# Kernel tuning notes

Hardware: AMD Instinct MI355X
Metric: run time of the kernel (lower is better)

Reference implementation:

```python
import math
import jax, jax.numpy as jnp
import numpy as np

H = 32          # query heads
KV = 8          # key/value heads (GQA)
D = 128         # head_dim
PAGE = 16       # Quest page size
TOPK = 256      # page budget
THETA = 10000.0


def _rope(x, pos):
    # x: [..., D]; llama rotate_half RoPE at scalar position pos
    half = D // 2
    inv = 1.0 / (THETA ** (jnp.arange(half, dtype=jnp.float32) * 2.0 / D))
    ang = pos * inv                                   # [half]
    cos = jnp.concatenate([jnp.cos(ang), jnp.cos(ang)])  # [D]
    sin = jnp.concatenate([jnp.sin(ang), jnp.sin(ang)])
    rot = jnp.concatenate([-x[..., half:], x[..., :half]], axis=-1)
    return x * cos + rot * sin


def setup_inputs() -> dict:
    key = jax.random.key(0)
    ks = jax.random.split(key, 7)
    hid = H * D
    s = 1.0 / math.sqrt(hid)
    return {
        "hidden_states": jax.random.normal(ks[0], (1, 1, hid), jnp.float32),
        "k_cache": jax.random.normal(ks[1], (32767, KV, D), jnp.float32),
        "v_cache": jax.random.normal(ks[2], (32767, KV, D), jnp.float32),
        "Wq": jax.random.normal(ks[3], (hid, H * D), jnp.float32) * s,
        "Wk": jax.random.normal(ks[4], (hid, KV * D), jnp.float32) * s,
        "Wv": jax.random.normal(ks[5], (hid, KV * D), jnp.float32) * s,
        "Wo": jax.random.normal(ks[6], (H * D, hid), jnp.float32) * s,
    }


def reference(hidden_states, k_cache, v_cache, Wq, Wk, Wv, Wo):
    x = hidden_states[0]                    # [1, hidden]
    q = (x @ Wq).reshape(H, D)              # decode: q_len == 1
    k = (x @ Wk).reshape(KV, D)
    v = (x @ Wv).reshape(KV, D)

    past = k_cache.shape[0]
    q = _rope(q, jnp.float32(past))
    k = _rope(k, jnp.float32(past))

    # append_kv: paged cache, seqlen = past + 1 = n_pages * PAGE
    Kc = jnp.concatenate([k_cache, k[None]], axis=0)   # [S, KV, D]
    Vc = jnp.concatenate([v_cache, v[None]], axis=0)
    S = past + 1
    n_pages = S // PAGE

    # decode_estimate: per-page min/max key metadata, Quest upper-bound score
    Kp = Kc.reshape(n_pages, PAGE, KV, D)
    kmax = Kp.max(axis=1)                   # [P, KV, D]
    kmin = Kp.min(axis=1)
    G = H // KV
    qh = q.reshape(KV, G, D)
    pmax = qh[None] * kmax[:, :, None, :]   # [P, KV, G, D]
    pmin = qh[None] * kmin[:, :, None, :]
    score = jnp.maximum(pmax, pmin).sum(-1) # [P, KV, G]
    score = score.reshape(n_pages, H).T     # [H, P]
    # most recent page always attended
    score = score.at[:, -1].set(jnp.inf)

    # decode_topk: per-head page selection
    _, pidx = jax.lax.top_k(score, TOPK)    # [H, TOPK]
    tok = (pidx[..., None] * PAGE + jnp.arange(PAGE)).reshape(H, -1)  # [H, T]

    # decode_sparse_attn: gather selected pages (GQA mapping) + attention
    kvmap = jnp.arange(H) // G              # query head -> kv head
    Ksel = Kc[tok, kvmap[:, None]]          # [H, T, D]
    Vsel = Vc[tok, kvmap[:, None]]
    att = jnp.einsum('hd,htd->ht', q, Ksel) * (1.0 / math.sqrt(D))
    w = jax.nn.softmax(att, axis=-1)
    out = jnp.einsum('ht,htd->hd', w, Vsel) # [H, D]

    y = out.reshape(1, H * D) @ Wo          # o_proj
    return y[None]                          # [1, 1, hidden]
```

## Files before the change

kernel.cpp:

```cpp
#include <hip/hip_runtime.h>
#include <math.h>

#define H 32
#define KV 8
#define D 128
#define PAGE 16
#define TOPK 256
#define NPAGES 2048
#define PAST 32767
#define HID 4096

#define WS_Q      0
#define WS_K      4096
#define WS_V      5120
#define WS_SCORES 6144
#define WS_PIDX   71680
#define WS_PART_M 79872
#define WS_PART_L 80896
#define WS_PART_O 81920
#define WS_ATTN   212992

#define NCHUNK 32
#define PPC    8

__global__ void qkv_kernel(const float* __restrict__ x,
                           const float* __restrict__ Wq,
                           const float* __restrict__ Wk,
                           const float* __restrict__ Wv,
                           float* __restrict__ ws) {
    __shared__ float xs[256];
    int tid = threadIdx.x;
    int rc = blockIdx.x / 24;
    int cg = blockIdx.x % 24;
    int r0 = rc * 256;
    xs[tid] = x[r0 + tid];
    __syncthreads();
    const float* W; int Cc; int col; float* dst;
    if (cg < 16)      { W = Wq; Cc = 4096; col = cg * 256 + tid;        dst = ws + WS_Q + col; }
    else if (cg < 20) { W = Wk; Cc = 1024; col = (cg - 16) * 256 + tid; dst = ws + WS_K + col; }
    else              { W = Wv; Cc = 1024; col = (cg - 20) * 256 + tid; dst = ws + WS_V + col; }
    const float* Wp = W + (size_t)r0 * Cc + col;
    float acc = 0.f;
#pragma unroll 8
    for (int r = 0; r < 256; ++r)
        acc = fmaf(xs[r], Wp[(size_t)r * Cc], acc);
    atomicAdd(dst, acc);
}

__global__ void rope_kernel(float* __restrict__ ws) {
    int idx = blockIdx.x * blockDim.x + threadIdx.x;
    if (idx >= 2560) return;
    float* base;
    if (idx < 2048) base = ws + WS_Q + (idx >> 6) * 128;
    else            base = ws + WS_K + ((idx - 2048) >> 6) * 128;
    int j = idx & 63;
    double t = (double)j / 64.0;
    float p = (float)pow(10000.0, t);
    float invf = 1.0f / p;
    float ang = 32767.0f * invf;
    float c = (float)cos((double)ang);
    float s = (float)sin((double)ang);
    float x0 = base[j], x1 = base[j + 64];
    base[j]      = x0 * c - x1 * s;
    base[j + 64] = x1 * c + x0 * s;
}

__global__ void score_kernel(const float* __restrict__ kc,
                             const float* __restrict__ q,
                             float* __restrict__ scores) {
    int tid = threadIdx.x;
    int lane = tid & 63;
    int wv = tid >> 6;
    int p = blockIdx.x >> 1;
    int kv = ((blockIdx.x & 1) << 2) + wv;
    const float* kp = kc + ((size_t)(p * PAGE) * KV + kv) * D + 2 * lane;
    float mx0 = -INFINITY, mx1 = -INFINITY, mn0 = INFINITY, mn1 = INFINITY;
#pragma unroll
    for (int t = 0; t < PAGE; ++t) {
        float2 v = *(const float2*)(kp + (size_t)t * (KV * D));
        mx0 = fmaxf(mx0, v.x); mn0 = fminf(mn0, v.x);
        mx1 = fmaxf(mx1, v.y); mn1 = fminf(mn1, v.y);
    }
    float sacc[4];
#pragma unroll
    for (int g = 0; g < 4; ++g) {
        int h = kv * 4 + g;
        float q0 = q[h * 128 + 2 * lane];
        float q1 = q[h * 128 + 2 * lane + 1];
        sacc[g] = fmaxf(q0 * mx0, q0 * mn0) + fmaxf(q1 * mx1, q1 * mn1);
    }
#pragma unroll
    for (int off = 32; off > 0; off >>= 1) {
#pragma unroll
        for (int g = 0; g < 4; ++g) sacc[g] += __shfl_xor(sacc[g], off);
    }
    if (lane == 0) {
#pragma unroll
        for (int g = 0; g < 4; ++g)
            scores[(size_t)(kv * 4 + g) * NPAGES + p] = sacc[g];
    }
}

__global__ void topk_kernel(const float* __restrict__ scores, int* __restrict__ pidx) {
    __shared__ unsigned su[NPAGES];
    __shared__ int hist[256];
    __shared__ int scan[256];
    __shared__ int wtot[4];
    __shared__ int cnt;
    __shared__ unsigned s_prefix;
    __shared__ int s_k;
    int tid = threadIdx.x;
    int lane = tid & 63;
    int wv = tid >> 6;
    int h = blockIdx.x;
    for (int i = tid; i < NPAGES; i += 256) {
        unsigned u;
        if (i == NPAGES - 1) u = 0xFFFFFFFFu;
        else {
            int b = __float_as_int(scores[(size_t)h * NPAGES + i]);
            u = (b >= 0) ? ((unsigned)b | 0x80000000u) : ~(unsigned)b;
        }
        su[i] = u;
    }
    if (tid == 0) cnt = 0;
    __syncthreads();

    unsigned prefix = 0;
    int K = TOPK;
    for (int level = 3; level >= 0; --level) {
        int shift = level * 8;
        unsigned pmask = (level == 3) ? 0u : (0xFFFFFFFFu << (shift + 8));
        hist[tid] = 0;
        __syncthreads();
        for (int i = tid; i < NPAGES; i += 256) {
            unsigned u = su[i];
            if ((u & pmask) == prefix)
                atomicAdd(&hist[(u >> shift) & 0xFF], 1);
        }
        __syncthreads();
        int v = hist[tid];
#pragma unroll
        for (int off = 1; off < 64; off <<= 1) {
            int o = __shfl_down(v, off);
            if (lane + off < 64) v += o;
        }
        if (lane == 0) wtot[wv] = v;
        __syncthreads();
        int add = 0;
        for (int w2 = wv + 1; w2 < 4; ++w2) add += wtot[w2];
        v += add;
        scan[tid] = v;
        __syncthreads();
        int nxt = (tid < 255) ? scan[tid + 1] : 0;
        if (v >= K && nxt < K) {
            s_prefix = prefix | ((unsigned)tid << shift);
            s_k = K - nxt;
        }
        __syncthreads();
        prefix = s_prefix;
        K = s_k;
        __syncthreads();
    }
    unsigned T = prefix;

    for (int i = tid; i < NPAGES; i += 256) {
        if (su[i] > T) {
            int pos = atomicAdd(&cnt, 1);
            pidx[h * TOPK + pos] = i;
        }
    }
    int base = TOPK - K;
    int i0 = tid * (NPAGES / 256);
    int tcount = 0;
#pragma unroll
    for (int j = 0; j < NPAGES / 256; ++j) if (su[i0 + j] == T) ++tcount;
    int sc = tcount;
#pragma unroll
    for (int off = 1; off < 64; off <<= 1) {
        int o = __shfl_up(sc, off);
        if (lane >= off) sc += o;
    }
    __syncthreads();
    if (lane == 63) wtot[wv] = sc;
    __syncthreads();
    int wadd = 0;
    for (int w2 = 0; w2 < wv; ++w2) wadd += wtot[w2];
    int pos = base + (sc - tcount) + wadd;
#pragma unroll
    for (int j = 0; j < NPAGES / 256; ++j) {
        if (su[i0 + j] == T) {
            if (pos < TOPK) pidx[h * TOPK + pos] = i0 + j;
            ++pos;
        }
    }
}

__global__ void attn_kernel(const float* __restrict__ kc,
                            const float* __restrict__ vc,
                            const float* __restrict__ ws,
                            const int* __restrict__ pidx,
                            float* __restrict__ part_m,
                            float* __restrict__ part_l,
                            float* __restrict__ part_o) {
    int tid = threadIdx.x;
    int lane = tid & 63;
    int wv = tid >> 6;
    int h = blockIdx.x >> 5;
    int c = blockIdx.x & 31;
    int kvh = h >> 2;
    __shared__ float qs[128];
    __shared__ float sm[4], sl[4];
    __shared__ float so[4 * 128];
    if (tid < 128) qs[tid] = ws[WS_Q + h * 128 + tid];
    __syncthreads();
    float q0 = qs[2 * lane], q1 = qs[2 * lane + 1];
    float m = -INFINITY, l = 0.f, o0 = 0.f, o1 = 0.f;
    const float scale = 0.08838834764831843f;
    for (int pi = 0; pi < 2; ++pi) {
        int page = pidx[h * TOPK + c * PPC + wv * 2 + pi];
        for (int t = 0; t < PAGE; ++t) {
            int tok = page * PAGE + t;
            const float *kp, *vp;
            if (tok == PAST) { kp = ws + WS_K + kvh * 128; vp = ws + WS_V + kvh * 128; }
            else {
                size_t off = ((size_t)tok * KV + kvh) * D;
                kp = kc + off; vp = vc + off;
            }
            float2 kk = *(const float2*)(kp + 2 * lane);
            float s = q0 * kk.x + q1 * kk.y;
#pragma unroll
            for (int off2 = 32; off2 > 0; off2 >>= 1) s += __shfl_xor(s, off2);
            s *= scale;
            float2 vvv = *(const float2*)(vp + 2 * lane);
            float nm = fmaxf(m, s);
            float rs = expf(m - nm);
            float w = expf(s - nm);
            l = l * rs + w;
            o0 = o0 * rs + w * vvv.x;
            o1 = o1 * rs + w * vvv.y;
            m = nm;
        }
    }
    if (lane == 0) { sm[wv] = m; sl[wv] = l; }
    so[wv * 128 + 2 * lane]     = o0;
    so[wv * 128 + 2 * lane + 1] = o1;
    __syncthreads();
    if (tid < 128) {
        float M = fmaxf(fmaxf(sm[0], sm[1]), fmaxf(sm[2], sm[3]));
        float L = 0.f, O = 0.f;
#pragma unroll
        for (int w2 = 0; w2 < 4; ++w2) {
            float f = expf(sm[w2] - M);
            L += f * sl[w2];
            O += f * so[w2 * 128 + tid];
        }
        int pc = h * NCHUNK + c;
        if (tid == 0) { part_m[pc] = M; part_l[pc] = L; }
        part_o[(size_t)pc * 128 + tid] = O;
    }
}

__global__ void combine_kernel(const float* __restrict__ part_m,
                               const float* __restrict__ part_l,
                               const float* __restrict__ part_o,
                               float* __restrict__ attn) {
    int h = blockIdx.x;
    int d = threadIdx.x;
    float M = -INFINITY;
    for (int c = 0; c < NCHUNK; ++c) M = fmaxf(M, part_m[h * NCHUNK + c]);
    float L = 0.f, O = 0.f;
    for (int c = 0; c < NCHUNK; ++c) {
        float f = expf(part_m[h * NCHUNK + c] - M);
        L += f * part_l[h * NCHUNK + c];
        O += f * part_o[(size_t)(h * NCHUNK + c) * 128 + d];
    }
    attn[h * 128 + d] = O / L;
}

__global__ void wo_kernel(const float* __restrict__ attn,
                          const float* __restrict__ Wo,
                          float* __restrict__ out) {
    __shared__ float xs[256];
    int tid = threadIdx.x;
    int rc = blockIdx.x >> 4;
    int cb = blockIdx.x & 15;
    int r0 = rc * 256;
    xs[tid] = attn[r0 + tid];
    __syncthreads();
    int col = cb * 256 + tid;
    const float* Wp = Wo + (size_t)r0 * 4096 + col;
    float acc = 0.f;
#pragma unroll 8
    for (int r = 0; r < 256; ++r)
        acc = fmaf(xs[r], Wp[(size_t)r * 4096], acc);
    atomicAdd(out + col, acc);
}

extern "C" void kernel_launch(void* const* d_in, const int* in_sizes, int n_in,
                              void* d_out, int out_size, void* d_ws, size_t ws_size,
                              hipStream_t stream) {
    const float* x  = (const float*)d_in[0];
    const float* kc = (const float*)d_in[1];
    const float* vc = (const float*)d_in[2];
    const float* Wq = (const float*)d_in[3];
    const float* Wk = (const float*)d_in[4];
    const float* Wv = (const float*)d_in[5];
    const float* Wo = (const float*)d_in[6];
    float* ws = (float*)d_ws;
    float* out = (float*)d_out;

    hipMemsetAsync(ws, 0, 6144 * sizeof(float), stream);
    hipMemsetAsync(out, 0, (size_t)out_size * sizeof(float), stream);

    qkv_kernel<<<384, 256, 0, stream>>>(x, Wq, Wk, Wv, ws);
    rope_kernel<<<10, 256, 0, stream>>>(ws);
    score_kernel<<<(NPAGES - 1) * 2, 256, 0, stream>>>(kc, ws + WS_Q, ws + WS_SCORES);
    topk_kernel<<<H, 256, 0, stream>>>(ws + WS_SCORES, (int*)(ws + WS_PIDX));
    attn_kernel<<<H * NCHUNK, 256, 0, stream>>>(kc, vc, ws, (const int*)(ws + WS_PIDX),
                                                ws + WS_PART_M, ws + WS_PART_L, ws + WS_PART_O);
    combine_kernel<<<H, 128, 0, stream>>>(ws + WS_PART_M, ws + WS_PART_L, ws + WS_PART_O,
                                          ws + WS_ATTN);
    wo_kernel<<<256, 256, 0, stream>>>(ws + WS_ATTN, Wo, out);
}
```

Measured before the change: 411.9 us.

## Vectorize GEMV, score and attention loads to float4 with restructured work split

The QKV and o_proj GEMV kernels switch to float4 weight loads, with each thread computing four columns over 64-row chunks, which changes the block decomposition. The score kernel reads keys as float4, with two half-waves covering alternate tokens that are merged by shuffle. The attention kernel gives each half-wave one page and replaces the online softmax with a two-pass score-then-accumulate over 16 tokens, combining 8 partials per block. The aim is wider memory transactions and shorter serial dependency chains, at the cost of more atomics per block and more registers. The launch configuration is not shown, so the grid sizes must match the new 6x64 and 4x64 block layouts.

```diff
diff --git a/kernel.cpp b/kernel.cpp
--- a/kernel.cpp
+++ b/kernel.cpp
@@ -28,23 +28,32 @@
                            const float* __restrict__ Wk,
                            const float* __restrict__ Wv,
                            float* __restrict__ ws) {
-    __shared__ float xs[256];
-    int tid = threadIdx.x;
-    int rc = blockIdx.x / 24;
-    int cg = blockIdx.x % 24;
-    int r0 = rc * 256;
-    xs[tid] = x[r0 + tid];
+    __shared__ float xs[64];
+    int tid = threadIdx.x;
+    int rc = blockIdx.x / 6;
+    int cg = blockIdx.x % 6;
+    int r0 = rc * 64;
+    if (tid < 64) xs[tid] = x[r0 + tid];
     __syncthreads();
     const float* W; int Cc; int col; float* dst;
-    if (cg < 16)      { W = Wq; Cc = 4096; col = cg * 256 + tid;        dst = ws + WS_Q + col; }
-    else if (cg < 20) { W = Wk; Cc = 1024; col = (cg - 16) * 256 + tid; dst = ws + WS_K + col; }
-    else              { W = Wv; Cc = 1024; col = (cg - 20) * 256 + tid; dst = ws + WS_V + col; }
+    if (cg < 4)       { W = Wq; Cc = 4096; col = cg * 1024 + tid * 4; dst = ws + WS_Q + col; }
+    else if (cg == 4) { W = Wk; Cc = 1024; col = tid * 4;             dst = ws + WS_K + col; }
+    else              { W = Wv; Cc = 1024; col = tid * 4;             dst = ws + WS_V + col; }
     const float* Wp = W + (size_t)r0 * Cc + col;
-    float acc = 0.f;
+    float4 acc = {0.f, 0.f, 0.f, 0.f};
 #pragma unroll 8
-    for (int r = 0; r < 256; ++r)
-        acc = fmaf(xs[r], Wp[(size_t)r * Cc], acc);
-    atomicAdd(dst, acc);
+    for (int r = 0; r < 64; ++r) {
+        float4 w4 = *(const float4*)(Wp + (size_t)r * Cc);
+        float xr = xs[r];
+        acc.x = fmaf(xr, w4.x, acc.x);
+        acc.y = fmaf(xr, w4.y, acc.y);
+        acc.z = fmaf(xr, w4.z, acc.z);
+        acc.w = fmaf(xr, w4.w, acc.w);
+    }
+    atomicAdd(dst + 0, acc.x);
+    atomicAdd(dst + 1, acc.y);
+    atomicAdd(dst + 2, acc.z);
+    atomicAdd(dst + 3, acc.w);
 }
 
 __global__ void rope_kernel(float* __restrict__ ws) {
@@ -71,26 +80,35 @@
     int tid = threadIdx.x;
     int lane = tid & 63;
     int wv = tid >> 6;
+    int sub = lane & 31;
+    int hf = lane >> 5;
     int p = blockIdx.x >> 1;
     int kv = ((blockIdx.x & 1) << 2) + wv;
-    const float* kp = kc + ((size_t)(p * PAGE) * KV + kv) * D + 2 * lane;
-    float mx0 = -INFINITY, mx1 = -INFINITY, mn0 = INFINITY, mn1 = INFINITY;
-#pragma unroll
-    for (int t = 0; t < PAGE; ++t) {
-        float2 v = *(const float2*)(kp + (size_t)t * (KV * D));
-        mx0 = fmaxf(mx0, v.x); mn0 = fminf(mn0, v.x);
-        mx1 = fmaxf(mx1, v.y); mn1 = fminf(mn1, v.y);
-    }
+    const float* kp0 = kc + ((size_t)(p * PAGE) * KV + kv) * D + 4 * sub;
+    float4 mx = {-INFINITY, -INFINITY, -INFINITY, -INFINITY};
+    float4 mn = { INFINITY,  INFINITY,  INFINITY,  INFINITY};
+#pragma unroll
+    for (int s8 = 0; s8 < 8; ++s8) {
+        int t = 2 * s8 + hf;
+        float4 v = *(const float4*)(kp0 + (size_t)t * (KV * D));
+        mx.x = fmaxf(mx.x, v.x); mn.x = fminf(mn.x, v.x);
+        mx.y = fmaxf(mx.y, v.y); mn.y = fminf(mn.y, v.y);
+        mx.z = fmaxf(mx.z, v.z); mn.z = fminf(mn.z, v.z);
+        mx.w = fmaxf(mx.w, v.w); mn.w = fminf(mn.w, v.w);
+    }
+    mx.x = fmaxf(mx.x, __shfl_xor(mx.x, 32)); mn.x = fminf(mn.x, __shfl_xor(mn.x, 32));
+    mx.y = fmaxf(mx.y, __shfl_xor(mx.y, 32)); mn.y = fminf(mn.y, __shfl_xor(mn.y, 32));
+    mx.z = fmaxf(mx.z, __shfl_xor(mx.z, 32)); mn.z = fminf(mn.z, __shfl_xor(mn.z, 32));
+    mx.w = fmaxf(mx.w, __shfl_xor(mx.w, 32)); mn.w = fminf(mn.w, __shfl_xor(mn.w, 32));
     float sacc[4];
 #pragma unroll
     for (int g = 0; g < 4; ++g) {
-        int h = kv * 4 + g;
-        float q0 = q[h * 128 + 2 * lane];
-        float q1 = q[h * 128 + 2 * lane + 1];
-        sacc[g] = fmaxf(q0 * mx0, q0 * mn0) + fmaxf(q1 * mx1, q1 * mn1);
-    }
-#pragma unroll
-    for (int off = 32; off > 0; off >>= 1) {
+        float4 qq = *(const float4*)(q + (size_t)(kv * 4 + g) * 128 + 4 * sub);
+        sacc[g] = fmaxf(qq.x * mx.x, qq.x * mn.x) + fmaxf(qq.y * mx.y, qq.y * mn.y)
+                + fmaxf(qq.z * mx.z, qq.z * mn.z) + fmaxf(qq.w * mx.w, qq.w * mn.w);
+    }
+#pragma unroll
+    for (int off = 16; off > 0; off >>= 1) {
 #pragma unroll
         for (int g = 0; g < 4; ++g) sacc[g] += __shfl_xor(sacc[g], off);
     }
@@ -205,51 +223,61 @@
     int tid = threadIdx.x;
     int lane = tid & 63;
     int wv = tid >> 6;
+    int sub = lane & 31;
+    int hf = lane >> 5;
     int h = blockIdx.x >> 5;
     int c = blockIdx.x & 31;
     int kvh = h >> 2;
     __shared__ float qs[128];
-    __shared__ float sm[4], sl[4];
-    __shared__ float so[4 * 128];
+    __shared__ float sm[8], sl[8];
+    __shared__ float so[8 * 128];
     if (tid < 128) qs[tid] = ws[WS_Q + h * 128 + tid];
     __syncthreads();
-    float q0 = qs[2 * lane], q1 = qs[2 * lane + 1];
-    float m = -INFINITY, l = 0.f, o0 = 0.f, o1 = 0.f;
+    float4 q4 = *(const float4*)(qs + 4 * sub);
+    int hidx = wv * 2 + hf;
+    int page = pidx[h * TOPK + c * PPC + hidx];
+    size_t base = ((size_t)(page * PAGE) * KV + kvh) * D + 4 * sub;
+    bool last = (page == NPAGES - 1);
     const float scale = 0.08838834764831843f;
-    for (int pi = 0; pi < 2; ++pi) {
-        int page = pidx[h * TOPK + c * PPC + wv * 2 + pi];
-        for (int t = 0; t < PAGE; ++t) {
-            int tok = page * PAGE + t;
-            const float *kp, *vp;
-            if (tok == PAST) { kp = ws + WS_K + kvh * 128; vp = ws + WS_V + kvh * 128; }
-            else {
-                size_t off = ((size_t)tok * KV + kvh) * D;
-                kp = kc + off; vp = vc + off;
-            }
-            float2 kk = *(const float2*)(kp + 2 * lane);
-            float s = q0 * kk.x + q1 * kk.y;
-#pragma unroll
-            for (int off2 = 32; off2 > 0; off2 >>= 1) s += __shfl_xor(s, off2);
-            s *= scale;
-            float2 vvv = *(const float2*)(vp + 2 * lane);
-            float nm = fmaxf(m, s);
-            float rs = expf(m - nm);
-            float w = expf(s - nm);
-            l = l * rs + w;
-            o0 = o0 * rs + w * vvv.x;
-            o1 = o1 * rs + w * vvv.y;
-            m = nm;
-        }
-    }
-    if (lane == 0) { sm[wv] = m; sl[wv] = l; }
-    so[wv * 128 + 2 * lane]     = o0;
-    so[wv * 128 + 2 * lane + 1] = o1;
+
+    float s[PAGE];
+#pragma unroll
+    for (int t = 0; t < PAGE; ++t) {
+        const float* kp = (last && t == PAGE - 1) ? (ws + WS_K + kvh * 128 + 4 * sub)
+                                                  : (kc + base + (size_t)t * (KV * D));
+        float4 kk = *(const float4*)kp;
+        float d = q4.x * kk.x + q4.y * kk.y + q4.z * kk.z + q4.w * kk.w;
+#pragma unroll
+        for (int off = 16; off > 0; off >>= 1) d += __shfl_xor(d, off);
+        s[t] = d * scale;
+    }
+    float m = -INFINITY;
+#pragma unroll
+    for (int t = 0; t < PAGE; ++t) m = fmaxf(m, s[t]);
+    float l = 0.f;
+    float4 o = {0.f, 0.f, 0.f, 0.f};
+#pragma unroll
+    for (int t = 0; t < PAGE; ++t) {
+        float w = expf(s[t] - m);
+        l += w;
+        const float* vp = (last && t == PAGE - 1) ? (ws + WS_V + kvh * 128 + 4 * sub)
+                                                  : (vc + base + (size_t)t * (KV * D));
+        float4 vv = *(const float4*)vp;
+        o.x = fmaf(w, vv.x, o.x);
+        o.y = fmaf(w, vv.y, o.y);
+        o.z = fmaf(w, vv.z, o.z);
+        o.w = fmaf(w, vv.w, o.w);
+    }
+    if (sub == 0) { sm[hidx] = m; sl[hidx] = l; }
+    *(float4*)(so + hidx * 128 + 4 * sub) = o;
     __syncthreads();
     if (tid < 128) {
-        float M = fmaxf(fmaxf(sm[0], sm[1]), fmaxf(sm[2], sm[3]));
+        float M = -INFINITY;
+#pragma unroll
+        for (int w2 = 0; w2 < 8; ++w2) M = fmaxf(M, sm[w2]);
         float L = 0.f, O = 0.f;
 #pragma unroll
-        for (int w2 = 0; w2 < 4; ++w2) {
+        for (int w2 = 0; w2 < 8; ++w2) {
             float f = expf(sm[w2] - M);
             L += f * sl[w2];
             O += f * so[w2 * 128 + tid];
@@ -280,20 +308,29 @@
 __global__ void wo_kernel(const float* __restrict__ attn,
                           const float* __restrict__ Wo,
                           float* __restrict__ out) {
-    __shared__ float xs[256];
-    int tid = threadIdx.x;
-    int rc = blockIdx.x >> 4;
-    int cb = blockIdx.x & 15;
-    int r0 = rc * 256;
-    xs[tid] = attn[r0 + tid];
-    __syncthreads();
-    int col = cb * 256 + tid;
+    __shared__ float xs[64];
+    int tid = threadIdx.x;
+    int rc = blockIdx.x >> 2;
+    int cb = blockIdx.x & 3;
+    int r0 = rc * 64;
+    if (tid < 64) xs[tid] = attn[r0 + tid];
+    __syncthreads();
+    int col = cb * 1024 + tid * 4;
     const float* Wp = Wo + (size_t)r0 * 4096 + col;
-    float acc = 0.f;
+    float4 acc = {0.f, 0.f, 0.f, 0.f};
 #pragma unroll 8
-    for (int r = 0; r < 256; ++r)
-        acc = fmaf(xs[r], Wp[(size_t)r * 4096], acc);
-    atomicAdd(out + col, acc);
+    for (int r = 0; r < 64; ++r) {
+        float4 w4 = *(const float4*)(Wp + (size_t)r * 4096);
+        float xr = xs[r];
+        acc.x = fmaf(xr, w4.x, acc.x);
+        acc.y = fmaf(xr, w4.y, acc.y);
+        acc.z = fmaf(xr, w4.z, acc.z);
+        acc.w = fmaf(xr, w4.w, acc.w);
+    }
+    atomicAdd(out + col + 0, acc.x);
+    atomicAdd(out + col + 1, acc.y);
+    atomicAdd(out + col + 2, acc.z);
+    atomicAdd(out + col + 3, acc.w);
 }
 
 extern "C" void kernel_launch(void* const* d_in, const int* in_sizes, int n_in,
```

Result: faster. 402.7 us (-2.2%).
